# Kernel optimization log

Measured on AMD Instinct MI355X. Metric: run time of the kernel, lower is better.

The kernel has to match this reference:

```python
import jax, jax.numpy as jnp
import numpy as np

HIDDEN = 768
INTER = 2048
N_EXPERTS = 8
TOP_K = 2
SWIGLU_LIMIT = 7.0
N_TOK = 8192


def setup_inputs() -> dict:
    key = jax.random.key(0)
    k_x, k_r, k_gu, k_d = jax.random.split(key, 4)
    x = jax.random.normal(k_x, (N_TOK, HIDDEN), dtype=jnp.float32)
    router_w = jax.random.normal(k_r, (N_EXPERTS, HIDDEN), dtype=jnp.float32) * 0.02
    gate_up_proj = jax.random.normal(k_gu, (N_EXPERTS, 2 * INTER, HIDDEN), dtype=jnp.float32) * 0.02
    down_proj = jax.random.normal(k_d, (N_EXPERTS, HIDDEN, INTER), dtype=jnp.float32) * 0.02
    return {"x": x, "router_w": router_w, "gate_up_proj": gate_up_proj, "down_proj": down_proj}


def reference(x, router_w, gate_up_proj, down_proj):
    # router: [n_tok, E]
    router_logits = x @ router_w.T
    topk_vals, topk_idx = jax.lax.top_k(router_logits, TOP_K)  # [n_tok, k]
    topk_weights = jax.nn.softmax(topk_vals.astype(jnp.float32), axis=-1).astype(x.dtype)

    out = jnp.zeros_like(x)
    # Loop over the small fixed expert set; each expert is a dense GEMM over all
    # tokens, masked by its per-token routing weight (0 for unrouted tokens) —
    # identical math to the original gather/GEMM/scatter dispatch.
    for e in range(N_EXPERTS):
        # per-token weight for expert e (sums slots; each expert appears at most once per token)
        w_e = jnp.sum(jnp.where(topk_idx == e, topk_weights, 0.0), axis=-1)  # [n_tok]
        gate_up = x @ gate_up_proj[e].T  # [n_tok, 2*I]
        gate, up = jnp.split(gate_up, 2, axis=-1)
        up = jnp.minimum(up, SWIGLU_LIMIT)
        mlp_out = (jax.nn.silu(gate) * up) @ down_proj[e].T  # [n_tok, H]
        out = out + mlp_out * w_e[:, None]
    return out
```

## Files before the change

kernel.cpp:

```cpp
#include <hip/hip_runtime.h>
#include <hip/hip_bf16.h>

typedef unsigned short u16;
typedef unsigned int u32;
typedef short bf16x8 __attribute__((ext_vector_type(8)));
typedef float f32x4 __attribute__((ext_vector_type(4)));

#define NTOK 8192
#define HID 768
#define INTER 2048
#define NEXP 8

#define MFMA16(a, b, c) __builtin_amdgcn_mfma_f32_16x16x32_bf16(a, b, c, 0, 0, 0)
#define S_BARRIER() __builtin_amdgcn_s_barrier()
#define WAITVM(n) asm volatile("s_waitcnt vmcnt(" #n ")" ::: "memory")

__device__ __forceinline__ u16 f2bf(float f) {
    u32 u = __builtin_bit_cast(u32, f);
    u32 r = (u + 0x7FFFu + ((u >> 16) & 1u)) >> 16;
    return (u16)r;
}

__device__ __forceinline__ void gld16(const void* g, void* l) {
    __builtin_amdgcn_global_load_lds((const __attribute__((address_space(1))) void*)g,
                                     (__attribute__((address_space(3))) void*)l, 16, 0, 0);
}

__global__ __launch_bounds__(256) void cvt_kernel(const float* __restrict__ src, u16* __restrict__ dst, int n8) {
    int i = blockIdx.x * blockDim.x + threadIdx.x;
    int stride = gridDim.x * blockDim.x;
    for (; i < n8; i += stride) {
        const float4* s = (const float4*)(src + (size_t)i * 8);
        float4 a = s[0], b = s[1];
        u16 r[8] = {f2bf(a.x), f2bf(a.y), f2bf(a.z), f2bf(a.w),
                    f2bf(b.x), f2bf(b.y), f2bf(b.z), f2bf(b.w)};
        *(uint4*)(dst + (size_t)i * 8) = *(const uint4*)r;
    }
}

__global__ __launch_bounds__(256) void router2z(const float* __restrict__ x, const float* __restrict__ rw,
                                                u32* __restrict__ route, float* __restrict__ wslot,
                                                float4* __restrict__ out4) {
    int wv = threadIdx.x >> 6, ln = threadIdx.x & 63;
    int t = blockIdx.x * 4 + wv;
    if (t >= NTOK) return;
    float4 z = {0.f, 0.f, 0.f, 0.f};
#pragma unroll
    for (int k = 0; k < 3; k++) out4[(size_t)t * 192 + ln + k * 64] = z;
    float xr[12];
#pragma unroll
    for (int j = 0; j < 12; j++) xr[j] = x[(size_t)t * HID + ln + j * 64];
    float lg[NEXP];
#pragma unroll
    for (int e = 0; e < NEXP; e++) {
        float a = 0.f;
#pragma unroll
        for (int j = 0; j < 12; j++) a += xr[j] * rw[e * HID + ln + j * 64];
#pragma unroll
        for (int off = 32; off; off >>= 1) a += __shfl_xor(a, off);
        lg[e] = a;
    }
    int i0 = 0;
    float v0 = lg[0];
#pragma unroll
    for (int e = 1; e < NEXP; e++)
        if (lg[e] > v0) { v0 = lg[e]; i0 = e; }
    int i1 = -1;
    float v1 = -1e30f;
#pragma unroll
    for (int e = 0; e < NEXP; e++) {
        if (e == i0) continue;
        if (lg[e] > v1) { v1 = lg[e]; i1 = e; }
    }
    float w0 = 1.f / (1.f + __expf(v1 - v0));
    float w1 = 1.f - w0;
    if (ln == 0) {
        wslot[0 * NTOK + t] = w0;
        wslot[1 * NTOK + t] = w1;
        route[t] = (u32)i0 | ((u32)i1 << 8);
    }
}

__global__ __launch_bounds__(1024) void scatter_kernel(const u32* __restrict__ route, int* __restrict__ counts,
                                                       int* __restrict__ tokslot, int* __restrict__ ntiles,
                                                       int* __restrict__ tiledesc, int* __restrict__ ebase) {
    __shared__ int sc[NEXP][1024];
    int tid = threadIdx.x;
    u32 rt[8];
    int cnt[NEXP] = {0, 0, 0, 0, 0, 0, 0, 0};
#pragma unroll
    for (int k = 0; k < 8; k++) {
        rt[k] = route[tid * 8 + k];
        cnt[rt[k] & 255]++;
        cnt[(rt[k] >> 8) & 255]++;
    }
#pragma unroll
    for (int e = 0; e < NEXP; e++) sc[e][tid] = cnt[e];
    __syncthreads();
    for (int off = 1; off < 1024; off <<= 1) {
        int v[NEXP];
#pragma unroll
        for (int e = 0; e < NEXP; e++) v[e] = (tid >= off) ? sc[e][tid - off] : 0;
        __syncthreads();
#pragma unroll
        for (int e = 0; e < NEXP; e++)
            if (tid >= off) sc[e][tid] += v[e];
        __syncthreads();
    }
    int base[NEXP];
#pragma unroll
    for (int e = 0; e < NEXP; e++) base[e] = sc[e][tid] - cnt[e];
#pragma unroll
    for (int k = 0; k < 8; k++) {
        int t = tid * 8 + k;
        int e0 = rt[k] & 255, e1 = (rt[k] >> 8) & 255;
        tokslot[e0 * NTOK + base[e0]] = t;
        base[e0]++;
        tokslot[e1 * NTOK + base[e1]] = t | (1 << 16);
        base[e1]++;
    }
    if (tid == 0) {
        int tot = 0, b = 0;
        for (int e = 0; e < NEXP; e++) {
            int c = sc[e][1023];
            counts[e] = c;
            ebase[e] = b;
            b += c;
            int nt = (c + 255) >> 8;
            for (int q = 0; q < nt; q++) tiledesc[tot++] = (e << 8) | q;
        }
        ntiles[0] = tot;
    }
}


#define STG(d, kt)                                           \
    do {                                                     \
        char* base_ = lds + (d)*24576 + (tid << 4);          \
        size_t ko_ = (size_t)(kt)*64;                        \
        gld16(aP[0] + ko_, base_);                           \
        gld16(aP[1] + ko_, base_ + 4096);                    \
        gld16(aP[2] + ko_, base_ + 8192);                    \
        gld16(aP[3] + ko_, base_ + 12288);                   \
        gld16(bP[0] + ko_, base_ + 16384);                   \
        gld16(bP[1] + ko_, base_ + 20480);                   \
    } while (0)

#define PIPE_MB(NKT)                                                      \
    f32x4 acc[8][4];                                                      \
    _Pragma("unroll") for (int m_ = 0; m_ < 8; m_++)                      \
        _Pragma("unroll") for (int n_ = 0; n_ < 4; n_++) acc[m_][n_] = (f32x4)0.f; \
    const int sOff = ((g4 ^ (rsel & 3) ^ ((rsel >> 2) & 3)) << 4);        \
    const int aBase = (wr * 128 + rsel) * 64 + sOff;                      \
    const int bBase = 16384 + (wc * 64 + rsel) * 64 + sOff;               \
    STG(0, 0);                                                            \
    WAITVM(0);                                                            \
    S_BARRIER();                                                          \
    for (int t = 0; t < (NKT); ++t) {                                     \
        if (t + 1 < (NKT)) STG((t + 1) & 1, t + 1);                       \
        const char* Tb = lds + (t & 1) * 24576;                           \
        bf16x8 af[8], bfr[4];                                             \
        _Pragma("unroll") for (int m_ = 0; m_ < 8; m_++)                  \
            af[m_] = *(const bf16x8*)(Tb + aBase + m_ * 1024);            \
        _Pragma("unroll") for (int n_ = 0; n_ < 4; n_++)                  \
            bfr[n_] = *(const bf16x8*)(Tb + bBase + n_ * 1024);           \
        _Pragma("unroll") for (int m_ = 0; m_ < 8; m_++)                  \
            _Pragma("unroll") for (int n_ = 0; n_ < 4; n_++)              \
                acc[m_][n_] = MFMA16(af[m_], bfr[n_], acc[m_][n_]);       \
        WAITVM(0);                                                        \
        S_BARRIER();                                                      \
    }

__global__ __launch_bounds__(256, 3) void gateup_mb(const u16* __restrict__ xb, const u16* __restrict__ gub,
                                                    const int* __restrict__ counts,
                                                    const int* __restrict__ ntiles, const int* __restrict__ tiledesc,
                                                    const int* __restrict__ tokslot, const int* __restrict__ ebase,
                                                    u16* __restrict__ h) {
    if ((int)blockIdx.y >= ntiles[0]) return;
    int td = tiledesc[blockIdx.y];
    int e = td >> 8;
    int cnt = counts[e];
    int eb = ebase[e];
    int row0 = (td & 255) * 256;
    int c0 = blockIdx.x * 64;

    extern __shared__ char lds[];
    int tid = threadIdx.x;
    int wv = tid >> 6, ln = tid & 63;
    int wr = wv >> 1, wc = wv & 1;
    int rsel = ln & 15, g4 = ln >> 4;

    int srow = tid >> 2, sl = tid & 3;
    int sswz = ((sl ^ (srow & 3) ^ ((srow >> 2) & 3)) << 4);
    const char* aP[4];
    const char* bP[2];
#pragma unroll
    for (int c = 0; c < 4; c++) {
        int gr = row0 + c * 64 + srow;
        gr = gr < cnt ? gr : cnt - 1;
        int tok = tokslot[e * NTOK + gr] & 0xFFFF;
        aP[c] = (const char*)xb + (size_t)tok * (HID * 2) + sswz;
    }
#pragma unroll
    for (int c = 0; c < 2; c++) {
        int r = c * 64 + srow;
        int wi = r & 63;
        int b = (wi >> 5) * 2048 + c0 + (r >> 6) * 32 + (wi & 31);
        bP[c] = (const char*)gub + ((size_t)e * 4096 + b) * (HID * 2) + sswz;
    }

    PIPE_MB(HID / 32)

#pragma unroll
    for (int mg = 0; mg < 8; mg++) {
#pragma unroll
        for (int j = 0; j < 4; j++) {
            int gr = row0 + wr * 128 + mg * 16 + g4 * 4 + j;
            if (gr >= cnt) continue;
            u16* hrow = h + (size_t)(eb + gr) * INTER;
#pragma unroll
            for (int n = 0; n < 2; n++) {
                float gv = acc[mg][n][j];
                float uv = fminf(acc[mg][n + 2][j], 7.0f);
                float sg = gv / (1.0f + __expf(-gv));
                hrow[c0 + wc * 32 + n * 16 + rsel] = f2bf(sg * uv);
            }
        }
    }
}

__global__ __launch_bounds__(256, 3) void down_mb(const u16* __restrict__ hb, const u16* __restrict__ dnb,
                                                  const int* __restrict__ counts,
                                                  const int* __restrict__ ntiles, const int* __restrict__ tiledesc,
                                                  const int* __restrict__ tokslot, const int* __restrict__ ebase,
                                                  const float* __restrict__ wslot, float* __restrict__ out) {
    if ((int)blockIdx.y >= ntiles[0]) return;
    int td = tiledesc[blockIdx.y];
    int e = td >> 8;
    int cnt = counts[e];
    int eb = ebase[e];
    int row0 = (td & 255) * 256;
    int col0 = blockIdx.x * 128;

    extern __shared__ char lds[];
    int tid = threadIdx.x;
    int wv = tid >> 6, ln = tid & 63;
    int wr = wv >> 1, wc = wv & 1;
    int rsel = ln & 15, g4 = ln >> 4;

    int srow = tid >> 2, sl = tid & 3;
    int sswz = ((sl ^ (srow & 3) ^ ((srow >> 2) & 3)) << 4);
    const char* aP[4];
    const char* bP[2];
#pragma unroll
    for (int c = 0; c < 4; c++) {
        int gr = row0 + c * 64 + srow;
        gr = gr < cnt ? gr : cnt - 1;
        aP[c] = (const char*)hb + (size_t)(eb + gr) * (INTER * 2) + sswz;
    }
#pragma unroll
    for (int c = 0; c < 2; c++) {
        int r = c * 64 + srow;
        bP[c] = (const char*)dnb + ((size_t)e * HID + col0 + r) * (INTER * 2) + sswz;
    }

    PIPE_MB(INTER / 32)

#pragma unroll
    for (int mg = 0; mg < 8; mg++) {
#pragma unroll
        for (int j = 0; j < 4; j++) {
            int gr = row0 + wr * 128 + mg * 16 + g4 * 4 + j;
            if (gr >= cnt) continue;
            int ts = tokslot[e * NTOK + gr];
            int tok = ts & 0xFFFF, slot = ts >> 16;
            float w = wslot[slot * NTOK + tok];
#pragma unroll
            for (int n = 0; n < 4; n++) {
                int col = col0 + wc * 64 + n * 16 + rsel;
                atomicAdd(&out[(size_t)tok * HID + col], w * acc[mg][n][j]);
            }
        }
    }
}

extern "C" void kernel_launch(void* const* d_in, const int* in_sizes, int n_in,
                              void* d_out, int out_size, void* d_ws, size_t ws_size,
                              hipStream_t stream) {
    const float* x = (const float*)d_in[0];
    const float* rw = (const float*)d_in[1];
    const float* gu = (const float*)d_in[2];
    const float* dn = (const float*)d_in[3];
    float* out = (float*)d_out;
    char* ws = (char*)d_ws;

    int* counts = (int*)(ws + 0);
    int* ntiles = (int*)(ws + 64);
    int* tiledesc = (int*)(ws + 128);
    int* ebase = (int*)(ws + 448);
    int* tokslot = (int*)(ws + 512);
    float* wslot = (float*)(ws + 262656);
    u16* xb = (u16*)(ws + 328192);
    u16* gub = (u16*)(ws + 12911104);
    u16* dnb = (u16*)(ws + 63242752);
    u16* hb = (u16*)(ws + 88408576);
    u32* route = (u32*)(ws + 88408576);

    cvt_kernel<<<2048, 256, 0, stream>>>(x, xb, NTOK * HID / 8);
    cvt_kernel<<<2048, 256, 0, stream>>>(gu, gub, NEXP * 2 * INTER * HID / 8);
    cvt_kernel<<<2048, 256, 0, stream>>>(dn, dnb, NEXP * HID * INTER / 8);
    router2z<<<NTOK / 4, 256, 0, stream>>>(x, rw, route, wslot, (float4*)out);
    scatter_kernel<<<1, 1024, 0, stream>>>(route, counts, tokslot, ntiles, tiledesc, ebase);
    gateup_mb<<<dim3(32, 72), 256, 49152, stream>>>(xb, gub, counts, ntiles, tiledesc, tokslot, ebase, hb);
    down_mb<<<dim3(6, 72), 256, 49152, stream>>>(hb, dnb, counts, ntiles, tiledesc, tokslot, ebase, wslot, out);
}
```

Before: 314.7 us.

## Split down-projection K dimension across two blocks and fuse conversion kernels

The down-projection kernel now launches twice as many blocks, and each block handles half of the INTER reduction, offset by 2048 bytes per half. Both halves atomically add their partial sums into the output. This raises the block count for the down GEMM, which previously had only 6x72 blocks, at the cost of doubling the atomic traffic to the output. Separately, the three fp32-to-bf16 conversion launches are merged into one kernel to cut launch overhead.

```diff
diff --git a/kernel.cpp b/kernel.cpp
--- a/kernel.cpp
+++ b/kernel.cpp
@@ -26,15 +26,24 @@
                                      (__attribute__((address_space(3))) void*)l, 16, 0, 0);
 }
 
-__global__ __launch_bounds__(256) void cvt_kernel(const float* __restrict__ src, u16* __restrict__ dst, int n8) {
+__global__ __launch_bounds__(256) void cvt3_kernel(const float* __restrict__ s0, u16* __restrict__ d0, int n0,
+                                                   const float* __restrict__ s1, u16* __restrict__ d1, int n1,
+                                                   const float* __restrict__ s2, u16* __restrict__ d2, int n2) {
     int i = blockIdx.x * blockDim.x + threadIdx.x;
     int stride = gridDim.x * blockDim.x;
-    for (; i < n8; i += stride) {
-        const float4* s = (const float4*)(src + (size_t)i * 8);
+    int ntot = n0 + n1 + n2;
+    for (; i < ntot; i += stride) {
+        const float* src;
+        u16* dst;
+        int k;
+        if (i < n0) { src = s0; dst = d0; k = i; }
+        else if (i < n0 + n1) { src = s1; dst = d1; k = i - n0; }
+        else { src = s2; dst = d2; k = i - n0 - n1; }
+        const float4* s = (const float4*)(src + (size_t)k * 8);
         float4 a = s[0], b = s[1];
         u16 r[8] = {f2bf(a.x), f2bf(a.y), f2bf(a.z), f2bf(a.w),
                     f2bf(b.x), f2bf(b.y), f2bf(b.z), f2bf(b.w)};
-        *(uint4*)(dst + (size_t)i * 8) = *(const uint4*)r;
+        *(uint4*)(dst + (size_t)k * 8) = *(const uint4*)r;
     }
 }
 
@@ -234,8 +243,10 @@
                                                   const int* __restrict__ ntiles, const int* __restrict__ tiledesc,
                                                   const int* __restrict__ tokslot, const int* __restrict__ ebase,
                                                   const float* __restrict__ wslot, float* __restrict__ out) {
-    if ((int)blockIdx.y >= ntiles[0]) return;
-    int td = tiledesc[blockIdx.y];
+    int slot = blockIdx.y;
+    if ((slot >> 1) >= ntiles[0]) return;
+    int td = tiledesc[slot >> 1];
+    int khalf = slot & 1;
     int e = td >> 8;
     int cnt = counts[e];
     int eb = ebase[e];
@@ -249,7 +260,7 @@
     int rsel = ln & 15, g4 = ln >> 4;
 
     int srow = tid >> 2, sl = tid & 3;
-    int sswz = ((sl ^ (srow & 3) ^ ((srow >> 2) & 3)) << 4);
+    int sswz = ((sl ^ (srow & 3) ^ ((srow >> 2) & 3)) << 4) + (khalf << 11);
     const char* aP[4];
     const char* bP[2];
 #pragma unroll
@@ -264,7 +275,7 @@
         bP[c] = (const char*)dnb + ((size_t)e * HID + col0 + r) * (INTER * 2) + sswz;
     }
 
-    PIPE_MB(INTER / 32)
+    PIPE_MB(INTER / 64)
 
 #pragma unroll
     for (int mg = 0; mg < 8; mg++) {
@@ -273,8 +284,8 @@
             int gr = row0 + wr * 128 + mg * 16 + g4 * 4 + j;
             if (gr >= cnt) continue;
             int ts = tokslot[e * NTOK + gr];
-            int tok = ts & 0xFFFF, slot = ts >> 16;
-            float w = wslot[slot * NTOK + tok];
+            int tok = ts & 0xFFFF, slotx = ts >> 16;
+            float w = wslot[slotx * NTOK + tok];
 #pragma unroll
             for (int n = 0; n < 4; n++) {
                 int col = col0 + wc * 64 + n * 16 + rsel;
@@ -306,11 +317,11 @@
     u16* hb = (u16*)(ws + 88408576);
     u32* route = (u32*)(ws + 88408576);
 
-    cvt_kernel<<<2048, 256, 0, stream>>>(x, xb, NTOK * HID / 8);
-    cvt_kernel<<<2048, 256, 0, stream>>>(gu, gub, NEXP * 2 * INTER * HID / 8);
-    cvt_kernel<<<2048, 256, 0, stream>>>(dn, dnb, NEXP * HID * INTER / 8);
+    cvt3_kernel<<<2048, 256, 0, stream>>>(x, xb, NTOK * HID / 8,
+                                          gu, gub, NEXP * 2 * INTER * HID / 8,
+                                          dn, dnb, NEXP * HID * INTER / 8);
     router2z<<<NTOK / 4, 256, 0, stream>>>(x, rw, route, wslot, (float4*)out);
     scatter_kernel<<<1, 1024, 0, stream>>>(route, counts, tokslot, ntiles, tiledesc, ebase);
     gateup_mb<<<dim3(32, 72), 256, 49152, stream>>>(xb, gub, counts, ntiles, tiledesc, tokslot, ebase, hb);
-    down_mb<<<dim3(6, 72), 256, 49152, stream>>>(hb, dnb, counts, ntiles, tiledesc, tokslot, ebase, wslot, out);
-}
+    down_mb<<<dim3(6, 144), 256, 49152, stream>>>(hb, dnb, counts, ntiles, tiledesc, tokslot, ebase, wslot, out);
+}
```

Result: slower. 363.5 us (+15.5%).

## Fuse weight conversions, fold x cast into router, retile down GEMM to 192 rows

Applied to the files above, without the earlier changes.

Merges the two weight fp32-to-bf16 conversion launches into one kernel. The x conversion moves into the router kernel, which already reads x, so x is read from memory once instead of twice. Token slots are packed compactly per expert and get a second tile list for the down projection. The down GEMM now uses 192-row tiles with a simpler two-stage LDS pipeline, which gives more blocks and less padding waste. The risk is that the hand-written down pipeline waits on every K step, which may expose more load latency than the shared macro did.

```diff
diff --git a/kernel.cpp b/kernel.cpp
--- a/kernel.cpp
+++ b/kernel.cpp
@@ -26,36 +26,52 @@
                                      (__attribute__((address_space(3))) void*)l, 16, 0, 0);
 }
 
-__global__ __launch_bounds__(256) void cvt_kernel(const float* __restrict__ src, u16* __restrict__ dst, int n8) {
+__global__ __launch_bounds__(256) void cvt2_kernel(const float* __restrict__ s1, u16* __restrict__ d1, int n1,
+                                                   const float* __restrict__ s2, u16* __restrict__ d2, int n2) {
     int i = blockIdx.x * blockDim.x + threadIdx.x;
     int stride = gridDim.x * blockDim.x;
-    for (; i < n8; i += stride) {
-        const float4* s = (const float4*)(src + (size_t)i * 8);
+    int ntot = n1 + n2;
+    for (; i < ntot; i += stride) {
+        const float* src;
+        u16* dst;
+        int k;
+        if (i < n1) { src = s1; dst = d1; k = i; }
+        else { src = s2; dst = d2; k = i - n1; }
+        const float4* s = (const float4*)(src + (size_t)k * 8);
         float4 a = s[0], b = s[1];
         u16 r[8] = {f2bf(a.x), f2bf(a.y), f2bf(a.z), f2bf(a.w),
                     f2bf(b.x), f2bf(b.y), f2bf(b.z), f2bf(b.w)};
-        *(uint4*)(dst + (size_t)i * 8) = *(const uint4*)r;
-    }
-}
-
-__global__ __launch_bounds__(256) void router2z(const float* __restrict__ x, const float* __restrict__ rw,
-                                                u32* __restrict__ route, float* __restrict__ wslot,
-                                                float4* __restrict__ out4) {
+        *(uint4*)(dst + (size_t)k * 8) = *(const uint4*)r;
+    }
+}
+
+__global__ __launch_bounds__(256) void router3(const float* __restrict__ x, const float* __restrict__ rw,
+                                               u32* __restrict__ route, float* __restrict__ wslot,
+                                               u32* __restrict__ xb32, float4* __restrict__ out4) {
     int wv = threadIdx.x >> 6, ln = threadIdx.x & 63;
     int t = blockIdx.x * 4 + wv;
     if (t >= NTOK) return;
     float4 z = {0.f, 0.f, 0.f, 0.f};
 #pragma unroll
     for (int k = 0; k < 3; k++) out4[(size_t)t * 192 + ln + k * 64] = z;
-    float xr[12];
-#pragma unroll
-    for (int j = 0; j < 12; j++) xr[j] = x[(size_t)t * HID + ln + j * 64];
+    const float2* x2 = (const float2*)(x + (size_t)t * HID);
+    float2 xr2[6];
+#pragma unroll
+    for (int j = 0; j < 6; j++) xr2[j] = x2[ln + 64 * j];
+    u32* xrow = xb32 + (size_t)t * (HID / 2);
+#pragma unroll
+    for (int j = 0; j < 6; j++)
+        xrow[ln + 64 * j] = (u32)f2bf(xr2[j].x) | ((u32)f2bf(xr2[j].y) << 16);
     float lg[NEXP];
 #pragma unroll
     for (int e = 0; e < NEXP; e++) {
+        const float2* rw2 = (const float2*)(rw + e * HID);
         float a = 0.f;
 #pragma unroll
-        for (int j = 0; j < 12; j++) a += xr[j] * rw[e * HID + ln + j * 64];
+        for (int j = 0; j < 6; j++) {
+            float2 r2 = rw2[ln + 64 * j];
+            a += xr2[j].x * r2.x + xr2[j].y * r2.y;
+        }
 #pragma unroll
         for (int off = 32; off; off >>= 1) a += __shfl_xor(a, off);
         lg[e] = a;
@@ -83,7 +99,8 @@
 
 __global__ __launch_bounds__(1024) void scatter_kernel(const u32* __restrict__ route, int* __restrict__ counts,
                                                        int* __restrict__ tokslot, int* __restrict__ ntiles,
-                                                       int* __restrict__ tiledesc, int* __restrict__ ebase) {
+                                                       int* __restrict__ tiledesc, int* __restrict__ ntiles2,
+                                                       int* __restrict__ tiledesc2, int* __restrict__ ebase) {
     __shared__ int sc[NEXP][1024];
     int tid = threadIdx.x;
     u32 rt[8];
@@ -107,6 +124,12 @@
             if (tid >= off) sc[e][tid] += v[e];
         __syncthreads();
     }
+    int ebL[NEXP];
+    {
+        int b = 0;
+#pragma unroll
+        for (int e = 0; e < NEXP; e++) { ebL[e] = b; b += sc[e][1023]; }
+    }
     int base[NEXP];
 #pragma unroll
     for (int e = 0; e < NEXP; e++) base[e] = sc[e][tid] - cnt[e];
@@ -114,22 +137,24 @@
     for (int k = 0; k < 8; k++) {
         int t = tid * 8 + k;
         int e0 = rt[k] & 255, e1 = (rt[k] >> 8) & 255;
-        tokslot[e0 * NTOK + base[e0]] = t;
+        tokslot[ebL[e0] + base[e0]] = t;
         base[e0]++;
-        tokslot[e1 * NTOK + base[e1]] = t | (1 << 16);
+        tokslot[ebL[e1] + base[e1]] = t | (1 << 16);
         base[e1]++;
     }
     if (tid == 0) {
-        int tot = 0, b = 0;
+        int tot = 0, tot2 = 0;
         for (int e = 0; e < NEXP; e++) {
             int c = sc[e][1023];
             counts[e] = c;
-            ebase[e] = b;
-            b += c;
+            ebase[e] = ebL[e];
             int nt = (c + 255) >> 8;
             for (int q = 0; q < nt; q++) tiledesc[tot++] = (e << 8) | q;
+            int nt2 = (c + 191) / 192;
+            for (int q = 0; q < nt2; q++) tiledesc2[tot2++] = (e << 8) | q;
         }
         ntiles[0] = tot;
+        ntiles2[0] = tot2;
     }
 }
 
@@ -198,7 +223,7 @@
     for (int c = 0; c < 4; c++) {
         int gr = row0 + c * 64 + srow;
         gr = gr < cnt ? gr : cnt - 1;
-        int tok = tokslot[e * NTOK + gr] & 0xFFFF;
+        int tok = tokslot[eb + gr] & 0xFFFF;
         aP[c] = (const char*)xb + (size_t)tok * (HID * 2) + sswz;
     }
 #pragma unroll
@@ -229,17 +254,28 @@
     }
 }
 
+#define DSTG(d, kt)                                          \
+    do {                                                     \
+        char* base_ = lds + (d)*20480 + (tid << 4);          \
+        size_t ko_ = (size_t)(kt)*64;                        \
+        gld16(aP[0] + ko_, base_);                           \
+        gld16(aP[1] + ko_, base_ + 4096);                    \
+        gld16(aP[2] + ko_, base_ + 8192);                    \
+        gld16(bP[0] + ko_, base_ + 12288);                   \
+        gld16(bP[1] + ko_, base_ + 16384);                   \
+    } while (0)
+
 __global__ __launch_bounds__(256, 3) void down_mb(const u16* __restrict__ hb, const u16* __restrict__ dnb,
                                                   const int* __restrict__ counts,
-                                                  const int* __restrict__ ntiles, const int* __restrict__ tiledesc,
+                                                  const int* __restrict__ ntiles2, const int* __restrict__ tiledesc2,
                                                   const int* __restrict__ tokslot, const int* __restrict__ ebase,
                                                   const float* __restrict__ wslot, float* __restrict__ out) {
-    if ((int)blockIdx.y >= ntiles[0]) return;
-    int td = tiledesc[blockIdx.y];
+    if ((int)blockIdx.y >= ntiles2[0]) return;
+    int td = tiledesc2[blockIdx.y];
     int e = td >> 8;
     int cnt = counts[e];
     int eb = ebase[e];
-    int row0 = (td & 255) * 256;
+    int row0 = (td & 255) * 192;
     int col0 = blockIdx.x * 128;
 
     extern __shared__ char lds[];
@@ -250,10 +286,10 @@
 
     int srow = tid >> 2, sl = tid & 3;
     int sswz = ((sl ^ (srow & 3) ^ ((srow >> 2) & 3)) << 4);
-    const char* aP[4];
+    const char* aP[3];
     const char* bP[2];
 #pragma unroll
-    for (int c = 0; c < 4; c++) {
+    for (int c = 0; c < 3; c++) {
         int gr = row0 + c * 64 + srow;
         gr = gr < cnt ? gr : cnt - 1;
         aP[c] = (const char*)hb + (size_t)(eb + gr) * (INTER * 2) + sswz;
@@ -264,15 +300,44 @@
         bP[c] = (const char*)dnb + ((size_t)e * HID + col0 + r) * (INTER * 2) + sswz;
     }
 
-    PIPE_MB(INTER / 32)
-
-#pragma unroll
-    for (int mg = 0; mg < 8; mg++) {
+    f32x4 acc[6][4];
+#pragma unroll
+    for (int m_ = 0; m_ < 6; m_++)
+#pragma unroll
+        for (int n_ = 0; n_ < 4; n_++) acc[m_][n_] = (f32x4)0.f;
+    const int sOff = ((g4 ^ (rsel & 3) ^ ((rsel >> 2) & 3)) << 4);
+    const int aBase = (wr * 96 + rsel) * 64 + sOff;
+    const int bBase = 12288 + (wc * 64 + rsel) * 64 + sOff;
+    DSTG(0, 0);
+    WAITVM(0);
+    S_BARRIER();
+    const int NKT = INTER / 32;
+    for (int t = 0; t < NKT; ++t) {
+        if (t + 1 < NKT) DSTG((t + 1) & 1, t + 1);
+        const char* Tb = lds + (t & 1) * 20480;
+        bf16x8 af[6], bfr[4];
+#pragma unroll
+        for (int m_ = 0; m_ < 6; m_++)
+            af[m_] = *(const bf16x8*)(Tb + aBase + m_ * 1024);
+#pragma unroll
+        for (int n_ = 0; n_ < 4; n_++)
+            bfr[n_] = *(const bf16x8*)(Tb + bBase + n_ * 1024);
+#pragma unroll
+        for (int m_ = 0; m_ < 6; m_++)
+#pragma unroll
+            for (int n_ = 0; n_ < 4; n_++)
+                acc[m_][n_] = MFMA16(af[m_], bfr[n_], acc[m_][n_]);
+        WAITVM(0);
+        S_BARRIER();
+    }
+
+#pragma unroll
+    for (int mg = 0; mg < 6; mg++) {
 #pragma unroll
         for (int j = 0; j < 4; j++) {
-            int gr = row0 + wr * 128 + mg * 16 + g4 * 4 + j;
+            int gr = row0 + wr * 96 + mg * 16 + g4 * 4 + j;
             if (gr >= cnt) continue;
-            int ts = tokslot[e * NTOK + gr];
+            int ts = tokslot[eb + gr];
             int tok = ts & 0xFFFF, slot = ts >> 16;
             float w = wslot[slot * NTOK + tok];
 #pragma unroll
@@ -296,21 +361,22 @@
 
     int* counts = (int*)(ws + 0);
     int* ntiles = (int*)(ws + 64);
-    int* tiledesc = (int*)(ws + 128);
-    int* ebase = (int*)(ws + 448);
-    int* tokslot = (int*)(ws + 512);
-    float* wslot = (float*)(ws + 262656);
-    u16* xb = (u16*)(ws + 328192);
-    u16* gub = (u16*)(ws + 12911104);
-    u16* dnb = (u16*)(ws + 63242752);
-    u16* hb = (u16*)(ws + 88408576);
-    u32* route = (u32*)(ws + 88408576);
-
-    cvt_kernel<<<2048, 256, 0, stream>>>(x, xb, NTOK * HID / 8);
-    cvt_kernel<<<2048, 256, 0, stream>>>(gu, gub, NEXP * 2 * INTER * HID / 8);
-    cvt_kernel<<<2048, 256, 0, stream>>>(dn, dnb, NEXP * HID * INTER / 8);
-    router2z<<<NTOK / 4, 256, 0, stream>>>(x, rw, route, wslot, (float4*)out);
-    scatter_kernel<<<1, 1024, 0, stream>>>(route, counts, tokslot, ntiles, tiledesc, ebase);
+    int* ntiles2 = (int*)(ws + 96);
+    int* ebase = (int*)(ws + 128);
+    int* tiledesc = (int*)(ws + 256);
+    int* tiledesc2 = (int*)(ws + 1024);
+    int* tokslot = (int*)(ws + 4096);
+    float* wslot = (float*)(ws + 69632);
+    u16* xb = (u16*)(ws + 135168);
+    u16* gub = (u16*)(ws + 12718080);
+    u16* dnb = (u16*)(ws + 63049728);
+    u16* hb = (u16*)(ws + 88215552);
+    u32* route = (u32*)(ws + 88215552);
+
+    cvt2_kernel<<<2048, 256, 0, stream>>>(gu, gub, NEXP * 2 * INTER * HID / 8,
+                                          dn, dnb, NEXP * HID * INTER / 8);
+    router3<<<NTOK / 4, 256, 0, stream>>>(x, rw, route, wslot, (u32*)xb, (float4*)out);
+    scatter_kernel<<<1, 1024, 0, stream>>>(route, counts, tokslot, ntiles, tiledesc, ntiles2, tiledesc2, ebase);
     gateup_mb<<<dim3(32, 72), 256, 49152, stream>>>(xb, gub, counts, ntiles, tiledesc, tokslot, ebase, hb);
-    down_mb<<<dim3(6, 72), 256, 49152, stream>>>(hb, dnb, counts, ntiles, tiledesc, tokslot, ebase, wslot, out);
-}
+    down_mb<<<dim3(6, 96), 256, 40960, stream>>>(hb, dnb, counts, ntiles2, tiledesc2, tokslot, ebase, wslot, out);
+}
```

New measurement: 331.7 us. 5.4% more time.
